# Kernel optimization log

Hardware: AMD Instinct MI355X
Metric: run time of the kernel (lower is better)

The kernel has to match this reference:

```python
import jax, jax.numpy as jnp
import numpy as np

B, IN, H, CTX = 16384, 1024, 1024, 2048


def setup_inputs() -> dict:
    key = jax.random.key(0)
    ks = jax.random.split(key, 20)
    stdv = 1.0 / np.sqrt(H)
    u = lambda k, shape: jax.random.uniform(k, shape, jnp.float32, -stdv, stdv)
    inp = {
        "y": jax.random.normal(ks[0], (B, IN), jnp.float32),
        "ctx": jax.random.normal(ks[1], (B, CTX), jnp.float32),
        "c0": jax.random.normal(ks[2], (B, H), jnp.float32),
        "h0": jax.random.normal(ks[3], (B, H), jnp.float32),
        # Concatenated gate weights in order (i, f, o, c), matching the
        # per-gate matrices Wi..Wc, Ui..Uc, Ci..Cc of the original module.
        "W": u(ks[4], (4 * H, IN)),   # input projections
        "U": u(ks[5], (4 * H, H)),    # hidden projections
        "C": u(ks[6], (4 * H, CTX)),  # context projections
        "b": u(ks[7], (4 * H,)),      # gate biases
    }
    return inp


def reference(y, ctx, c0, h0, W, U, C, b):
    # One fused GEMM per input stream instead of 12 small ones; same math.
    gates = y @ W.T + h0 @ U.T + ctx @ C.T + b  # [B, 4H]
    gi, gf, go, gc = jnp.split(gates, 4, axis=-1)
    i = jax.nn.sigmoid(gi)
    f = jax.nn.sigmoid(gf)
    o = jax.nn.sigmoid(go)
    c_hat = jnp.tanh(gc)
    c = i * c_hat + f * c0
    h = o * jnp.tanh(c)
    return (c, h)
```

## Files before the change

### kernel.cpp

```cpp
#include <hip/hip_runtime.h>
#include <hip/hip_bf16.h>
#include <stdint.h>

typedef __attribute__((ext_vector_type(8))) short short8;
typedef __attribute__((ext_vector_type(8))) unsigned short ushort8;
typedef __attribute__((ext_vector_type(4))) float f32x4;
typedef __attribute__((ext_vector_type(8))) __bf16 bf16x8;

#define GAS __attribute__((address_space(1)))
#define LAS __attribute__((address_space(3)))

static constexpr int Bn = 16384;
static constexpr int Hn = 1024;
static constexpr int KT = 4096;
static constexpr int NT = KT / 64;

#define SBAR()   __builtin_amdgcn_s_barrier()
#define VMCNT(n) asm volatile("s_waitcnt vmcnt(" #n ")" ::: "memory")
#define FENCE()  asm volatile("" ::: "memory")

__device__ __forceinline__ unsigned short f2bf(float f) {
  unsigned u = __builtin_bit_cast(unsigned, f);
  u = (u + 0x7FFFu + ((u >> 16) & 1u)) >> 16;
  return (unsigned short)u;
}

__device__ __forceinline__ float fast_sigm(float x) {
  return __builtin_amdgcn_rcpf(1.f + __expf(-x));
}
__device__ __forceinline__ float fast_tanh(float x) {
  return 1.f - 2.f * __builtin_amdgcn_rcpf(__expf(2.f * x) + 1.f);
}

__global__ __launch_bounds__(256) void cvt_concat_k(
    const float* __restrict__ s0, const float* __restrict__ s1,
    const float* __restrict__ s2, unsigned short* __restrict__ dst,
    long long n8) {
  long long stride = (long long)gridDim.x * blockDim.x;
  for (long long g = (long long)blockIdx.x * blockDim.x + threadIdx.x; g < n8;
       g += stride) {
    long long row = g >> 9;
    int cg = (int)(g & 511) << 3;
    const float* src;
    if (cg < 1024)      src = s0 + row * 1024 + cg;
    else if (cg < 2048) src = s1 + row * 1024 + (cg - 1024);
    else                src = s2 + row * 2048 + (cg - 2048);
    float4 f0 = *(const float4*)src;
    float4 f1 = *(const float4*)(src + 4);
    ushort8 o;
    o[0] = f2bf(f0.x); o[1] = f2bf(f0.y); o[2] = f2bf(f0.z); o[3] = f2bf(f0.w);
    o[4] = f2bf(f1.x); o[5] = f2bf(f1.y); o[6] = f2bf(f1.z); o[7] = f2bf(f1.w);
    *(ushort8*)(dst + (g << 3)) = o;
  }
}

__global__ __launch_bounds__(256) void cvt_pack_w(
    const float* __restrict__ s0, const float* __restrict__ s1,
    const float* __restrict__ s2, unsigned short* __restrict__ dst,
    long long ntot) {
  long long stride = (long long)gridDim.x * blockDim.x;
  for (long long g = (long long)blockIdx.x * blockDim.x + threadIdx.x; g < ntot;
       g += stride) {
    int li = (int)(g & 63);
    long long rec = g >> 6;
    int cb = (int)(rec & 255);
    int k32 = (int)(rec >> 8);
    int fr = li & 15, ksl = li >> 4;
    int row = cb * 16 + fr;
    int k0 = k32 * 32 + ksl * 8;
    const float* src;
    if (k0 < 1024)      src = s0 + (size_t)row * 1024 + k0;
    else if (k0 < 2048) src = s1 + (size_t)row * 1024 + (k0 - 1024);
    else                src = s2 + (size_t)row * 2048 + (k0 - 2048);
    float4 f0 = *(const float4*)src;
    float4 f1 = *(const float4*)(src + 4);
    ushort8 o;
    o[0] = f2bf(f0.x); o[1] = f2bf(f0.y); o[2] = f2bf(f0.z); o[3] = f2bf(f0.w);
    o[4] = f2bf(f1.x); o[5] = f2bf(f1.y); o[6] = f2bf(f1.z); o[7] = f2bf(f1.w);
    *(ushort8*)(dst + (g << 3)) = o;
  }
}

__global__ __launch_bounds__(512, 2) void lstm_gemm(
    const unsigned short* __restrict__ X, const unsigned short* __restrict__ Wp,
    const float* __restrict__ bias, const float* __restrict__ c0,
    float* __restrict__ out_c, float* __restrict__ out_h) {
  extern __shared__ char smem[];

  int bid = blockIdx.x;
  int swz = (bid & 7) * 128 + (bid >> 3);
  int mblk = swz >> 4, cblk = swz & 15;
  int brow0 = mblk * 256;
  int hcol0 = cblk * 64;

  int tid = threadIdx.x;
  int lane = tid & 63, wid = tid >> 6;
  int wr = wid >> 2, wc = wid & 3;

  const char* Xc = (const char*)X;
  const char* Wpc = (const char*)Wp;

  int rr = tid >> 3;
  uint32_t cbyte = (uint32_t)(((tid & 7) * 16) ^ ((rr & 7) << 4));
  uint32_t aoffj[4];
#pragma unroll
  for (int j = 0; j < 4; ++j)
    aoffj[j] = (uint32_t)(brow0 + j * 64 + rr) * (KT * 2) + cbyte;

  auto stage_A = [&](int tt, int dbuf) {
    int ts = tt < NT ? tt : NT - 1;
#pragma unroll
    for (int j = 0; j < 4; ++j) {
      const char* src = Xc + aoffj[j] + (uint32_t)ts * 128u;
      char* dst = smem + dbuf * 32768 + j * 8192 + wid * 1024;
      __builtin_amdgcn_global_load_lds((const GAS unsigned int*)src,
                                       (LAS unsigned int*)dst, 16, 0, 0);
    }
  };

  int kg = (lane >> 4) << 4;
  int sw = (lane & 7) << 4;
  int koff0 = kg ^ sw;
  int koff1 = (64 + kg) ^ sw;
  int fr = lane & 15;

  const char* bbp[4];
#pragma unroll
  for (int n = 0; n < 4; ++n) {
    int cb = n * 64 + cblk * 4 + wc;
    bbp[n] = Wpc + ((size_t)cb * 64 + lane) * 16;
  }

  f32x4 acc[8][4] = {};
  short8 bfrE[4][2], bfrO[4][2];

  stage_A(0, 0);
  FENCE();
#pragma unroll
  for (int n = 0; n < 4; ++n) {
    bfrE[n][0] = *(const short8*)(bbp[n]);
    bfrE[n][1] = *(const short8*)(bbp[n] + 262144);
  }
  stage_A(1, 1);

  int bufA = 0;

#define TILE(T_, BC, BN)                                                      \
  {                                                                           \
    VMCNT(12);                                                                \
    SBAR();                                                                   \
    int pb = bufA * 32768;                                                    \
    int stg = bufA + 2; if (stg >= 3) stg -= 3;                               \
    _Pragma("unroll")                                                         \
    for (int q = 0; q < 4; ++q) {                                             \
      int ab = pb + ((2 * q + wr) * 32 + fr) * 128;                           \
      short8 a0 = *(const short8*)(smem + ab + koff0);                        \
      short8 a1 = *(const short8*)(smem + ab + koff1);                        \
      short8 a2 = *(const short8*)(smem + ab + 2048 + koff0);                 \
      short8 a3 = *(const short8*)(smem + ab + 2048 + koff1);                 \
      if (q == 1) {          \
        int ts = (T_) + 1 < NT ? (T_) + 1 : NT - 1;                           \
        size_t tb = (size_t)(2 * ts) * 262144u;                               \
        _Pragma("unroll")                                                     \
        for (int n = 0; n < 4; ++n) {                                         \
          BN[n][0] = *(const short8*)(bbp[n] + tb);                           \
          BN[n][1] = *(const short8*)(bbp[n] + tb + 262144);                  \
        }                                                                     \
      }                                                                       \
      if (q == 3) stage_A((T_) + 2, stg);                                     \
      __builtin_amdgcn_s_setprio(1);                                          \
      _Pragma("unroll")                                                       \
      for (int n = 0; n < 4; ++n) {                                           \
        acc[2 * q][n] = __builtin_amdgcn_mfma_f32_16x16x32_bf16(              \
            __builtin_bit_cast(bf16x8, a0), __builtin_bit_cast(bf16x8, BC[n][0]),\
            acc[2 * q][n], 0, 0, 0);                                          \
        acc[2 * q + 1][n] = __builtin_amdgcn_mfma_f32_16x16x32_bf16(          \
            __builtin_bit_cast(bf16x8, a2), __builtin_bit_cast(bf16x8, BC[n][0]),\
            acc[2 * q + 1][n], 0, 0, 0);                                      \
      }                                                                       \
      _Pragma("unroll")                                                       \
      for (int n = 0; n < 4; ++n) {                                           \
        acc[2 * q][n] = __builtin_amdgcn_mfma_f32_16x16x32_bf16(              \
            __builtin_bit_cast(bf16x8, a1), __builtin_bit_cast(bf16x8, BC[n][1]),\
            acc[2 * q][n], 0, 0, 0);                                          \
        acc[2 * q + 1][n] = __builtin_amdgcn_mfma_f32_16x16x32_bf16(          \
            __builtin_bit_cast(bf16x8, a3), __builtin_bit_cast(bf16x8, BC[n][1]),\
            acc[2 * q + 1][n], 0, 0, 0);                                      \
      }                                                                       \
      __builtin_amdgcn_s_setprio(0);                                          \
    }                                                                         \
    bufA = bufA + 1; if (bufA >= 3) bufA = 0;                                 \
  }

  for (int t = 0; t < NT; t += 2) {
    TILE(t, bfrE, bfrO)
    TILE(t + 1, bfrO, bfrE)
  }
#undef TILE

  int col = hcol0 + wc * 16 + fr;
  float bi = bias[col], bf_ = bias[1024 + col];
  float bo = bias[2048 + col], bc = bias[3072 + col];
#pragma unroll
  for (int m = 0; m < 8; ++m) {
    int row0 = brow0 + (2 * (m >> 1) + wr) * 32 + (m & 1) * 16 + ((lane >> 4) << 2);
#pragma unroll
    for (int j = 0; j < 4; ++j) {
      size_t idx = (size_t)(row0 + j) * 1024 + col;
      float i_ = fast_sigm(acc[m][0][j] + bi);
      float f_ = fast_sigm(acc[m][1][j] + bf_);
      float o_ = fast_sigm(acc[m][2][j] + bo);
      float ch = fast_tanh(acc[m][3][j] + bc);
      float cn = i_ * ch + f_ * c0[idx];
      out_c[idx] = cn;
      out_h[idx] = o_ * fast_tanh(cn);
    }
  }
}

__global__ __launch_bounds__(256) void lstm_naive(
    const float* __restrict__ y, const float* __restrict__ ctx,
    const float* __restrict__ c0, const float* __restrict__ h0,
    const float* __restrict__ W, const float* __restrict__ U,
    const float* __restrict__ C, const float* __restrict__ b,
    float* __restrict__ out_c, float* __restrict__ out_h) {
  size_t t = (size_t)blockIdx.x * blockDim.x + threadIdx.x;
  if (t >= (size_t)Bn * Hn) return;
  int row = (int)(t >> 10), col = (int)(t & 1023);
  float g[4];
#pragma unroll
  for (int gg = 0; gg < 4; ++gg) {
    int wrow = gg * 1024 + col;
    float s = b[wrow];
    const float* yr = y + (size_t)row * 1024;
    const float* Wr = W + (size_t)wrow * 1024;
    for (int k = 0; k < 1024; ++k) s += yr[k] * Wr[k];
    const float* hr = h0 + (size_t)row * 1024;
    const float* Ur = U + (size_t)wrow * 1024;
    for (int k = 0; k < 1024; ++k) s += hr[k] * Ur[k];
    const float* cr = ctx + (size_t)row * 2048;
    const float* Cr = C + (size_t)wrow * 2048;
    for (int k = 0; k < 2048; ++k) s += cr[k] * Cr[k];
    g[gg] = s;
  }
  float i_ = fast_sigm(g[0]), f_ = fast_sigm(g[1]);
  float o_ = fast_sigm(g[2]), ch = fast_tanh(g[3]);
  float cn = i_ * ch + f_ * c0[t];
  out_c[t] = cn;
  out_h[t] = o_ * fast_tanh(cn);
}

extern "C" void kernel_launch(void* const* d_in, const int* in_sizes, int n_in,
                              void* d_out, int out_size, void* d_ws, size_t ws_size,
                              hipStream_t stream) {
  const float* y   = (const float*)d_in[0];
  const float* ctx = (const float*)d_in[1];
  const float* c0  = (const float*)d_in[2];
  const float* h0  = (const float*)d_in[3];
  const float* W   = (const float*)d_in[4];
  const float* U   = (const float*)d_in[5];
  const float* C   = (const float*)d_in[6];
  const float* b   = (const float*)d_in[7];
  float* out = (float*)d_out;
  float* out_c = out;
  float* out_h = out + (size_t)Bn * Hn;

  const size_t needX = (size_t)Bn * KT * 2;
  const size_t needW = (size_t)(4 * Hn) * KT * 2;

  if (ws_size >= needX + needW) {
    unsigned short* Xb = (unsigned short*)d_ws;
    unsigned short* Wb = (unsigned short*)((char*)d_ws + needX);
    cvt_concat_k<<<2048, 256, 0, stream>>>(y, h0, ctx, Xb, (long long)Bn * 512);
    cvt_pack_w<<<2048, 256, 0, stream>>>(W, U, C, Wb,
                                         (long long)(4 * Hn) * KT / 8);
    (void)hipFuncSetAttribute((const void*)lstm_gemm,
                              hipFuncAttributeMaxDynamicSharedMemorySize, 98304);
    lstm_gemm<<<1024, 512, 98304, stream>>>(Xb, Wb, b, c0, out_c, out_h);
  } else {
    lstm_naive<<<(Bn * Hn + 255) / 256, 256, 0, stream>>>(y, ctx, c0, h0, W, U, C,
                                                          b, out_c, out_h);
  }
}
```

Measured before the change: 556.7 us.

## Use 1024-thread blocks with 16 waves, halving per-wave accumulator tile

Each block now runs 1024 threads (16 waves, 4 row-waves x 4 column-waves) instead of 512, so every wave owns 64 rows x 64 gate-columns and half as many accumulators. The even/odd double-buffered B-fragment registers are replaced by a single set reloaded at the end of each k-tile, and the A-stage load is split into two wide chunks. The aim is lower register pressure and more waves in flight to hide latency. The cost is that each B fragment is reused across fewer MFMAs, and the B loads are no longer overlapped with compute. With 96KB LDS per block, the requested 4 blocks per CU likely cannot all fit.

```diff
diff --git a/kernel.cpp b/kernel.cpp
--- a/kernel.cpp
+++ b/kernel.cpp
@@ -81,7 +81,7 @@
   }
 }
 
-__global__ __launch_bounds__(512, 2) void lstm_gemm(
+__global__ __launch_bounds__(1024, 4) void lstm_gemm(
     const unsigned short* __restrict__ X, const unsigned short* __restrict__ Wp,
     const float* __restrict__ bias, const float* __restrict__ c0,
     float* __restrict__ out_c, float* __restrict__ out_h) {
@@ -102,17 +102,17 @@
 
   int rr = tid >> 3;
   uint32_t cbyte = (uint32_t)(((tid & 7) * 16) ^ ((rr & 7) << 4));
-  uint32_t aoffj[4];
-#pragma unroll
-  for (int j = 0; j < 4; ++j)
-    aoffj[j] = (uint32_t)(brow0 + j * 64 + rr) * (KT * 2) + cbyte;
+  uint32_t aoffj[2];
+#pragma unroll
+  for (int j = 0; j < 2; ++j)
+    aoffj[j] = (uint32_t)(brow0 + j * 128 + rr) * (KT * 2) + cbyte;
 
   auto stage_A = [&](int tt, int dbuf) {
     int ts = tt < NT ? tt : NT - 1;
 #pragma unroll
-    for (int j = 0; j < 4; ++j) {
+    for (int j = 0; j < 2; ++j) {
       const char* src = Xc + aoffj[j] + (uint32_t)ts * 128u;
-      char* dst = smem + dbuf * 32768 + j * 8192 + wid * 1024;
+      char* dst = smem + dbuf * 32768 + j * 16384 + wid * 1024;
       __builtin_amdgcn_global_load_lds((const GAS unsigned int*)src,
                                        (LAS unsigned int*)dst, 16, 0, 0);
     }
@@ -131,79 +131,65 @@
     bbp[n] = Wpc + ((size_t)cb * 64 + lane) * 16;
   }
 
-  f32x4 acc[8][4] = {};
-  short8 bfrE[4][2], bfrO[4][2];
+  f32x4 acc[4][4] = {};
+  short8 bfr[4][2];
 
   stage_A(0, 0);
   FENCE();
 #pragma unroll
   for (int n = 0; n < 4; ++n) {
-    bfrE[n][0] = *(const short8*)(bbp[n]);
-    bfrE[n][1] = *(const short8*)(bbp[n] + 262144);
-  }
+    bfr[n][0] = *(const short8*)(bbp[n]);
+    bfr[n][1] = *(const short8*)(bbp[n] + 262144);
+  }
+  FENCE();
   stage_A(1, 1);
 
   int bufA = 0;
 
-#define TILE(T_, BC, BN)                                                      \
-  {                                                                           \
-    VMCNT(12);                                                                \
-    SBAR();                                                                   \
-    int pb = bufA * 32768;                                                    \
-    int stg = bufA + 2; if (stg >= 3) stg -= 3;                               \
-    _Pragma("unroll")                                                         \
-    for (int q = 0; q < 4; ++q) {                                             \
-      int ab = pb + ((2 * q + wr) * 32 + fr) * 128;                           \
-      short8 a0 = *(const short8*)(smem + ab + koff0);                        \
-      short8 a1 = *(const short8*)(smem + ab + koff1);                        \
-      short8 a2 = *(const short8*)(smem + ab + 2048 + koff0);                 \
-      short8 a3 = *(const short8*)(smem + ab + 2048 + koff1);                 \
-      if (q == 1) {          \
-        int ts = (T_) + 1 < NT ? (T_) + 1 : NT - 1;                           \
-        size_t tb = (size_t)(2 * ts) * 262144u;                               \
-        _Pragma("unroll")                                                     \
-        for (int n = 0; n < 4; ++n) {                                         \
-          BN[n][0] = *(const short8*)(bbp[n] + tb);                           \
-          BN[n][1] = *(const short8*)(bbp[n] + tb + 262144);                  \
-        }                                                                     \
-      }                                                                       \
-      if (q == 3) stage_A((T_) + 2, stg);                                     \
-      __builtin_amdgcn_s_setprio(1);                                          \
-      _Pragma("unroll")                                                       \
-      for (int n = 0; n < 4; ++n) {                                           \
-        acc[2 * q][n] = __builtin_amdgcn_mfma_f32_16x16x32_bf16(              \
-            __builtin_bit_cast(bf16x8, a0), __builtin_bit_cast(bf16x8, BC[n][0]),\
-            acc[2 * q][n], 0, 0, 0);                                          \
-        acc[2 * q + 1][n] = __builtin_amdgcn_mfma_f32_16x16x32_bf16(          \
-            __builtin_bit_cast(bf16x8, a2), __builtin_bit_cast(bf16x8, BC[n][0]),\
-            acc[2 * q + 1][n], 0, 0, 0);                                      \
-      }                                                                       \
-      _Pragma("unroll")                                                       \
-      for (int n = 0; n < 4; ++n) {                                           \
-        acc[2 * q][n] = __builtin_amdgcn_mfma_f32_16x16x32_bf16(              \
-            __builtin_bit_cast(bf16x8, a1), __builtin_bit_cast(bf16x8, BC[n][1]),\
-            acc[2 * q][n], 0, 0, 0);                                          \
-        acc[2 * q + 1][n] = __builtin_amdgcn_mfma_f32_16x16x32_bf16(          \
-            __builtin_bit_cast(bf16x8, a3), __builtin_bit_cast(bf16x8, BC[n][1]),\
-            acc[2 * q + 1][n], 0, 0, 0);                                      \
-      }                                                                       \
-      __builtin_amdgcn_s_setprio(0);                                          \
-    }                                                                         \
-    bufA = bufA + 1; if (bufA >= 3) bufA = 0;                                 \
-  }
-
-  for (int t = 0; t < NT; t += 2) {
-    TILE(t, bfrE, bfrO)
-    TILE(t + 1, bfrO, bfrE)
-  }
-#undef TILE
+  for (int t = 0; t < NT; ++t) {
+    VMCNT(10);
+    SBAR();
+    int pb = bufA * 32768;
+    int stg = bufA + 2; if (stg >= 3) stg -= 3;
+#pragma unroll
+    for (int m = 0; m < 4; ++m) {
+      int ab = pb + ((wr * 4 + m) * 16 + fr) * 128;
+      short8 a0 = *(const short8*)(smem + ab + koff0);
+      short8 a1 = *(const short8*)(smem + ab + koff1);
+      __builtin_amdgcn_s_setprio(1);
+#pragma unroll
+      for (int n = 0; n < 4; ++n)
+        acc[m][n] = __builtin_amdgcn_mfma_f32_16x16x32_bf16(
+            __builtin_bit_cast(bf16x8, a0), __builtin_bit_cast(bf16x8, bfr[n][0]),
+            acc[m][n], 0, 0, 0);
+#pragma unroll
+      for (int n = 0; n < 4; ++n)
+        acc[m][n] = __builtin_amdgcn_mfma_f32_16x16x32_bf16(
+            __builtin_bit_cast(bf16x8, a1), __builtin_bit_cast(bf16x8, bfr[n][1]),
+            acc[m][n], 0, 0, 0);
+      __builtin_amdgcn_s_setprio(0);
+    }
+    {
+      int ts = t + 1 < NT ? t + 1 : NT - 1;
+      size_t tb = (size_t)(2 * ts) * 262144u;
+      FENCE();
+#pragma unroll
+      for (int n = 0; n < 4; ++n) {
+        bfr[n][0] = *(const short8*)(bbp[n] + tb);
+        bfr[n][1] = *(const short8*)(bbp[n] + tb + 262144);
+      }
+      FENCE();
+    }
+    stage_A(t + 2, stg);
+    bufA = bufA + 1; if (bufA >= 3) bufA = 0;
+  }
 
   int col = hcol0 + wc * 16 + fr;
   float bi = bias[col], bf_ = bias[1024 + col];
   float bo = bias[2048 + col], bc = bias[3072 + col];
 #pragma unroll
-  for (int m = 0; m < 8; ++m) {
-    int row0 = brow0 + (2 * (m >> 1) + wr) * 32 + (m & 1) * 16 + ((lane >> 4) << 2);
+  for (int m = 0; m < 4; ++m) {
+    int row0 = brow0 + (wr * 4 + m) * 16 + ((lane >> 4) << 2);
 #pragma unroll
     for (int j = 0; j < 4; ++j) {
       size_t idx = (size_t)(row0 + j) * 1024 + col;
@@ -276,7 +262,7 @@
                                          (long long)(4 * Hn) * KT / 8);
     (void)hipFuncSetAttribute((const void*)lstm_gemm,
                               hipFuncAttributeMaxDynamicSharedMemorySize, 98304);
-    lstm_gemm<<<1024, 512, 98304, stream>>>(Xb, Wb, b, c0, out_c, out_h);
+    lstm_gemm<<<1024, 1024, 98304, stream>>>(Xb, Wb, b, c0, out_c, out_h);
   } else {
     lstm_naive<<<(Bn * Hn + 255) / 256, 256, 0, stream>>>(y, ctx, c0, h0, W, U, C,
                                                           b, out_c, out_h);
```

New measurement: 759.1 us. 1.36x slower.

## Prefetch c0 tile into LDS during tail pipeline slots and split B loads

Applied to the files above, without the earlier changes.

The two final pipeline stages, which used to re-stage a clamped, redundant A tile, now use async global-to-LDS loads to bring the block's c0 tile into the freed LDS buffers. The epilogue reads c0 from shared memory instead of issuing scattered global loads after the GEMM. The B-fragment prefetch is also split across two sub-iterations to spread out register pressure and memory issue. An added wait and barrier before the epilogue make sure the c0 data has landed, and the epilogue LDS reads may hit bank conflicts.

```diff
diff --git a/kernel.cpp b/kernel.cpp
--- a/kernel.cpp
+++ b/kernel.cpp
@@ -107,14 +107,28 @@
   for (int j = 0; j < 4; ++j)
     aoffj[j] = (uint32_t)(brow0 + j * 64 + rr) * (KT * 2) + cbyte;
 
-  auto stage_A = [&](int tt, int dbuf) {
-    int ts = tt < NT ? tt : NT - 1;
-#pragma unroll
-    for (int j = 0; j < 4; ++j) {
-      const char* src = Xc + aoffj[j] + (uint32_t)ts * 128u;
-      char* dst = smem + dbuf * 32768 + j * 8192 + wid * 1024;
-      __builtin_amdgcn_global_load_lds((const GAS unsigned int*)src,
-                                       (LAS unsigned int*)dst, 16, 0, 0);
+  auto stage_slot = [&](int tt, int dbuf) {
+    if (tt < NT) {
+#pragma unroll
+      for (int j = 0; j < 4; ++j) {
+        const char* src = Xc + aoffj[j] + (uint32_t)tt * 128u;
+        char* dst = smem + dbuf * 32768 + j * 8192 + wid * 1024;
+        __builtin_amdgcn_global_load_lds((const GAS unsigned int*)src,
+                                         (LAS unsigned int*)dst, 16, 0, 0);
+      }
+    } else {
+      int chunk = tt - NT;
+      int base = chunk ? 65536 : 32768;
+#pragma unroll
+      for (int j = 0; j < 4; ++j) {
+        int srow = chunk * 128 + j * 32 + (tid >> 4);
+        int scol = (tid & 15) * 4;
+        const char* src =
+            (const char*)(c0 + (size_t)(brow0 + srow) * 1024 + hcol0 + scol);
+        char* dst = smem + base + j * 8192 + wid * 1024;
+        __builtin_amdgcn_global_load_lds((const GAS unsigned int*)src,
+                                         (LAS unsigned int*)dst, 16, 0, 0);
+      }
     }
   };
 
@@ -134,14 +148,14 @@
   f32x4 acc[8][4] = {};
   short8 bfrE[4][2], bfrO[4][2];
 
-  stage_A(0, 0);
+  stage_slot(0, 0);
   FENCE();
 #pragma unroll
   for (int n = 0; n < 4; ++n) {
     bfrE[n][0] = *(const short8*)(bbp[n]);
     bfrE[n][1] = *(const short8*)(bbp[n] + 262144);
   }
-  stage_A(1, 1);
+  stage_slot(1, 1);
 
   int bufA = 0;
 
@@ -158,16 +172,21 @@
       short8 a1 = *(const short8*)(smem + ab + koff1);                        \
       short8 a2 = *(const short8*)(smem + ab + 2048 + koff0);                 \
       short8 a3 = *(const short8*)(smem + ab + 2048 + koff1);                 \
-      if (q == 1) {          \
+      if (q == 1) {                                   \
         int ts = (T_) + 1 < NT ? (T_) + 1 : NT - 1;                           \
         size_t tb = (size_t)(2 * ts) * 262144u;                               \
         _Pragma("unroll")                                                     \
-        for (int n = 0; n < 4; ++n) {                                         \
+        for (int n = 0; n < 4; ++n)                                           \
           BN[n][0] = *(const short8*)(bbp[n] + tb);                           \
+      }                                                                       \
+      if (q == 2) {                                   \
+        int ts = (T_) + 1 < NT ? (T_) + 1 : NT - 1;                           \
+        size_t tb = (size_t)(2 * ts) * 262144u;                               \
+        _Pragma("unroll")                                                     \
+        for (int n = 0; n < 4; ++n)                                           \
           BN[n][1] = *(const short8*)(bbp[n] + tb + 262144);                  \
-        }                                                                     \
       }                                                                       \
-      if (q == 3) stage_A((T_) + 2, stg);                                     \
+      if (q == 3) stage_slot((T_) + 2, stg);                                  \
       __builtin_amdgcn_s_setprio(1);                                          \
       _Pragma("unroll")                                                       \
       for (int n = 0; n < 4; ++n) {                                           \
@@ -198,20 +217,26 @@
   }
 #undef TILE
 
+  VMCNT(0);
+  SBAR();
+
   int col = hcol0 + wc * 16 + fr;
   float bi = bias[col], bf_ = bias[1024 + col];
   float bo = bias[2048 + col], bc = bias[3072 + col];
 #pragma unroll
   for (int m = 0; m < 8; ++m) {
-    int row0 = brow0 + (2 * (m >> 1) + wr) * 32 + (m & 1) * 16 + ((lane >> 4) << 2);
+    int rrel0 = (2 * (m >> 1) + wr) * 32 + (m & 1) * 16 + ((lane >> 4) << 2);
 #pragma unroll
     for (int j = 0; j < 4; ++j) {
-      size_t idx = (size_t)(row0 + j) * 1024 + col;
+      int r = rrel0 + j;
+      size_t idx = (size_t)(brow0 + r) * 1024 + col;
+      float c0v = *(const float*)(smem + 32768 + (r >> 7) * 32768 +
+                                  (r & 127) * 256 + (wc * 16 + fr) * 4);
       float i_ = fast_sigm(acc[m][0][j] + bi);
       float f_ = fast_sigm(acc[m][1][j] + bf_);
       float o_ = fast_sigm(acc[m][2][j] + bo);
       float ch = fast_tanh(acc[m][3][j] + bc);
-      float cn = i_ * ch + f_ * c0[idx];
+      float cn = i_ * ch + f_ * c0v;
       out_c[idx] = cn;
       out_h[idx] = o_ * fast_tanh(cn);
     }
```

After: 593.4 us. 1.07x slower.

## Make GEMM blocks persistent over four M-tiles with cross-tile prefetch

Applied to the files above, without the earlier changes.

Cuts the launch from 1024 to 256 blocks, so each block handles four consecutive 256-row M tiles for one column block. The A and B prefetch pipeline runs straight across tile boundaries, with the next tile's first K slices staged during the previous tile's tail, and the epilogue runs inline between tiles. This is meant to remove pipeline fill and drain and block launch overhead at tile boundaries. In exchange there is less parallelism: 256 blocks on a chip with about 256 CUs gives one block per CU despite launch bounds allowing two, and the epilogue stalls the pipeline between tiles.

```diff
diff --git a/kernel.cpp b/kernel.cpp
--- a/kernel.cpp
+++ b/kernel.cpp
@@ -88,9 +88,9 @@
   extern __shared__ char smem[];
 
   int bid = blockIdx.x;
-  int swz = (bid & 7) * 128 + (bid >> 3);
-  int mblk = swz >> 4, cblk = swz & 15;
-  int brow0 = mblk * 256;
+  int swz = (bid & 7) * 32 + (bid >> 3);
+  int cblk = swz >> 4;
+  int mgroup = swz & 15;
   int hcol0 = cblk * 64;
 
   int tid = threadIdx.x;
@@ -102,16 +102,18 @@
 
   int rr = tid >> 3;
   uint32_t cbyte = (uint32_t)(((tid & 7) * 16) ^ ((rr & 7) << 4));
-  uint32_t aoffj[4];
-#pragma unroll
-  for (int j = 0; j < 4; ++j)
-    aoffj[j] = (uint32_t)(brow0 + j * 64 + rr) * (KT * 2) + cbyte;
-
-  auto stage_A = [&](int tt, int dbuf) {
-    int ts = tt < NT ? tt : NT - 1;
+  uint32_t aoffj[4], aoffjN[4];
+#pragma unroll
+  for (int j = 0; j < 4; ++j) {
+    aoffj[j] = (uint32_t)(mgroup * 1024 + j * 64 + rr) * 8192u + cbyte;
+    aoffjN[j] = aoffj[j] + (256u * 8192u);
+  }
+
+  auto stage_A = [&](int ts, int nxt, int dbuf) {
 #pragma unroll
     for (int j = 0; j < 4; ++j) {
-      const char* src = Xc + aoffj[j] + (uint32_t)ts * 128u;
+      uint32_t off = (nxt ? aoffjN[j] : aoffj[j]) + (uint32_t)ts * 128u;
+      const char* src = Xc + off;
       char* dst = smem + dbuf * 32768 + j * 8192 + wid * 1024;
       __builtin_amdgcn_global_load_lds((const GAS unsigned int*)src,
                                        (LAS unsigned int*)dst, 16, 0, 0);
@@ -134,18 +136,18 @@
   f32x4 acc[8][4] = {};
   short8 bfrE[4][2], bfrO[4][2];
 
-  stage_A(0, 0);
+  stage_A(0, 0, 0);
   FENCE();
 #pragma unroll
   for (int n = 0; n < 4; ++n) {
     bfrE[n][0] = *(const short8*)(bbp[n]);
     bfrE[n][1] = *(const short8*)(bbp[n] + 262144);
   }
-  stage_A(1, 1);
+  stage_A(1, 0, 1);
 
   int bufA = 0;
 
-#define TILE(T_, BC, BN)                                                      \
+#define TILE(T_, G_, BC, BN)                                                  \
   {                                                                           \
     VMCNT(12);                                                                \
     SBAR();                                                                   \
@@ -158,16 +160,20 @@
       short8 a1 = *(const short8*)(smem + ab + koff1);                        \
       short8 a2 = *(const short8*)(smem + ab + 2048 + koff0);                 \
       short8 a3 = *(const short8*)(smem + ab + 2048 + koff1);                 \
-      if (q == 1) {          \
-        int ts = (T_) + 1 < NT ? (T_) + 1 : NT - 1;                           \
-        size_t tb = (size_t)(2 * ts) * 262144u;                               \
+      if (q == 1) {              \
+        int gt1 = (G_)*NT + (T_) + 1;                                         \
+        int tsb = gt1 < 4 * NT ? (gt1 & 63) : 63;                             \
+        size_t tb = (size_t)(2 * tsb) * 262144u;                              \
         _Pragma("unroll")                                                     \
         for (int n = 0; n < 4; ++n) {                                         \
           BN[n][0] = *(const short8*)(bbp[n] + tb);                           \
           BN[n][1] = *(const short8*)(bbp[n] + tb + 262144);                  \
         }                                                                     \
       }                                                                       \
-      if (q == 3) stage_A((T_) + 2, stg);                                     \
+      if (q == 3) {         \
+        int tp2 = (T_) + 2;                                                   \
+        stage_A(tp2 & 63, tp2 >= NT ? 1 : 0, stg);                            \
+      }                                                                       \
       __builtin_amdgcn_s_setprio(1);                                          \
       _Pragma("unroll")                                                       \
       for (int n = 0; n < 4; ++n) {                                           \
@@ -192,30 +198,47 @@
     bufA = bufA + 1; if (bufA >= 3) bufA = 0;                                 \
   }
 
-  for (int t = 0; t < NT; t += 2) {
-    TILE(t, bfrE, bfrO)
-    TILE(t + 1, bfrO, bfrE)
+  for (int g = 0; g < 4; ++g) {
+    for (int t = 0; t < NT; t += 2) {
+      TILE(t, g, bfrE, bfrO)
+      TILE(t + 1, g, bfrO, bfrE)
+    }
+
+    int brow0 = (mgroup * 4 + g) * 256;
+    int col = hcol0 + wc * 16 + fr;
+    float bi = bias[col], bf_ = bias[1024 + col];
+    float bo = bias[2048 + col], bc = bias[3072 + col];
+#pragma unroll
+    for (int m = 0; m < 8; ++m) {
+      int row0 =
+          brow0 + (2 * (m >> 1) + wr) * 32 + (m & 1) * 16 + ((lane >> 4) << 2);
+#pragma unroll
+      for (int j = 0; j < 4; ++j) {
+        size_t idx = (size_t)(row0 + j) * 1024 + col;
+        float i_ = fast_sigm(acc[m][0][j] + bi);
+        float f_ = fast_sigm(acc[m][1][j] + bf_);
+        float o_ = fast_sigm(acc[m][2][j] + bo);
+        float ch = fast_tanh(acc[m][3][j] + bc);
+        float cn = i_ * ch + f_ * c0[idx];
+        out_c[idx] = cn;
+        out_h[idx] = o_ * fast_tanh(cn);
+      }
+    }
+
+#pragma unroll
+    for (int m = 0; m < 8; ++m)
+#pragma unroll
+      for (int n = 0; n < 4; ++n)
+#pragma unroll
+        for (int j = 0; j < 4; ++j) acc[m][n][j] = 0.f;
+
+#pragma unroll
+    for (int j = 0; j < 4; ++j) {
+      aoffj[j] = aoffjN[j];
+      if (g < 2) aoffjN[j] += 256u * 8192u;
+    }
   }
 #undef TILE
-
-  int col = hcol0 + wc * 16 + fr;
-  float bi = bias[col], bf_ = bias[1024 + col];
-  float bo = bias[2048 + col], bc = bias[3072 + col];
-#pragma unroll
-  for (int m = 0; m < 8; ++m) {
-    int row0 = brow0 + (2 * (m >> 1) + wr) * 32 + (m & 1) * 16 + ((lane >> 4) << 2);
-#pragma unroll
-    for (int j = 0; j < 4; ++j) {
-      size_t idx = (size_t)(row0 + j) * 1024 + col;
-      float i_ = fast_sigm(acc[m][0][j] + bi);
-      float f_ = fast_sigm(acc[m][1][j] + bf_);
-      float o_ = fast_sigm(acc[m][2][j] + bo);
-      float ch = fast_tanh(acc[m][3][j] + bc);
-      float cn = i_ * ch + f_ * c0[idx];
-      out_c[idx] = cn;
-      out_h[idx] = o_ * fast_tanh(cn);
-    }
-  }
 }
 
 __global__ __launch_bounds__(256) void lstm_naive(
@@ -276,7 +299,7 @@
                                          (long long)(4 * Hn) * KT / 8);
     (void)hipFuncSetAttribute((const void*)lstm_gemm,
                               hipFuncAttributeMaxDynamicSharedMemorySize, 98304);
-    lstm_gemm<<<1024, 512, 98304, stream>>>(Xb, Wb, b, c0, out_c, out_h);
+    lstm_gemm<<<256, 512, 98304, stream>>>(Xb, Wb, b, c0, out_c, out_h);
   } else {
     lstm_naive<<<(Bn * Hn + 255) / 256, 256, 0, stream>>>(y, ctx, c0, h0, W, U, C,
                                                           b, out_c, out_h);
```

Result: no change. 556.2 us (median of 3 runs) (-0.1%).
